# Performance work log

Measured on AMD Instinct MI355X. Metric: run time of the kernel, lower is better.

The kernel has to match this reference:

```python
import jax, jax.numpy as jnp
import numpy as np

N = 1 << 20  # total rows
D = 64       # feature dim
HALF = N // 2


def setup_inputs() -> dict:
    key = jax.random.key(0)
    k_data, k_part, k_perm = jax.random.split(key, 3)
    data = jax.random.normal(k_data, (N, D), dtype=jnp.float32)
    # exactly HALF zeros and HALF ones, randomly interleaved -> static partition sizes
    labels = jnp.concatenate([jnp.zeros(HALF, jnp.int32), jnp.ones(HALF, jnp.int32)])
    partitions = jax.random.permutation(k_part, labels)
    # destination rows: a random permutation of [0, N) split between the two partitions
    perm = jax.random.permutation(k_perm, jnp.arange(N, dtype=jnp.int32))
    index0 = perm[:HALF]
    index1 = perm[HALF:]
    return {"data": data, "partitions": partitions, "index0": index0, "index1": index1}


def reference(data, partitions, index0, index1):
    n0 = index0.shape[0]  # static size of partition 0 (by construction)
    # dynamic_partition: stable sort by label puts partition-0 rows (in original
    # order) first, then partition-1 rows (in original order).
    order = jnp.argsort(partitions, stable=True)  # [N] gather indices
    part0 = data[order[:n0]]   # rows with partitions == 0, original order
    part1 = data[order[n0:]]   # rows with partitions == 1, original order
    # dynamic_stitch: out[index0[i]] = part0[i]; out[index1[j]] = part1[j]
    out = jnp.zeros((n0 + index1.shape[0], data.shape[1]), dtype=data.dtype)
    out = out.at[index0].set(part0)
    out = out.at[index1].set(part1)
    return out
```

## Files before the change

### kernel.cpp

```cpp
#include <hip/hip_runtime.h>

#define GROUP 256

typedef float f4 __attribute__((ext_vector_type(4)));

__global__ __launch_bounds__(256)
void dps_count(const int* __restrict__ parts, int n, int* __restrict__ group_sums) {
    const int t = threadIdx.x;
    const int w = t >> 6;
    const int n4 = n >> 2;
    const int4* p4 = reinterpret_cast<const int4*>(parts);
    #pragma unroll
    for (int it = 0; it < 16; ++it) {
        int i4 = blockIdx.x * 4096 + it * 256 + t;
        int s = 0;
        if (i4 < n4) {
            int4 v = p4[i4];
            s = v.x + v.y + v.z + v.w;
        }
        #pragma unroll
        for (int off = 32; off >= 1; off >>= 1) s += __shfl_down(s, off, 64);
        if ((t & 63) == 0) {
            int g = blockIdx.x * 64 + it * 4 + w;
            int ngroups = (n + GROUP - 1) / GROUP;
            if (g < ngroups) group_sums[g] = s;
        }
    }
}

__global__ __launch_bounds__(256)
void dps_scan(int* __restrict__ gs, int nb) {
    __shared__ int lds[256];
    const int t = threadIdx.x;
    int v[16];
    int s = 0;
    #pragma unroll
    for (int k = 0; k < 16; ++k) {
        int idx = t * 16 + k;
        v[k] = (idx < nb) ? gs[idx] : 0;
        s += v[k];
    }
    lds[t] = s;
    __syncthreads();
    for (int off = 1; off < 256; off <<= 1) {
        int add = (t >= off) ? lds[t - off] : 0;
        __syncthreads();
        lds[t] += add;
        __syncthreads();
    }
    int run = lds[t] - s;
    #pragma unroll
    for (int k = 0; k < 16; ++k) {
        int idx = t * 16 + k;
        if (idx < nb) gs[idx] = run;
        run += v[k];
    }
}

__global__ __launch_bounds__(256)
void dps_fused(const f4* __restrict__ data4,
               const int* __restrict__ parts,
               const int* __restrict__ index0,
               const int* __restrict__ index1,
               const int* __restrict__ group_excl,
               int n,
               f4* __restrict__ out4) {
    __shared__ int lds [256];
    __shared__ int ldsd[256];
    const int t    = threadIdx.x;
    const int base = blockIdx.x * GROUP;
    const int i    = base + t;

    int p = (i < n) ? parts[i] : 0;
    lds[t] = p;
    __syncthreads();
    for (int off = 1; off < 256; off <<= 1) {
        int add = (t >= off) ? lds[t - off] : 0;
        __syncthreads();
        lds[t] += add;
        __syncthreads();
    }
    int ones_excl = group_excl[blockIdx.x] + (lds[t] - p);
    if (i < n) {
        ldsd[t] = p ? index1[ones_excl] : index0[i - ones_excl];
    }
    __syncthreads();

    const f4* src = data4 + ((long)base << 4);
    const int q  = t & 15;
    const int r0 = t >> 4;
    if (base + GROUP <= n) {
        #pragma unroll
        for (int it = 0; it < 16; ++it) {
            int r = it * 16 + r0;
            f4 v = __builtin_nontemporal_load(src + (r << 4) + q);
            long dr = (long)ldsd[r];
            __builtin_nontemporal_store(v, out4 + (dr << 4) + q);
        }
    } else {
        for (int it = 0; it < 16; ++it) {
            int r = it * 16 + r0;
            if (base + r < n) {
                f4 v = src[(r << 4) + q];
                out4[((long)ldsd[r] << 4) + q] = v;
            }
        }
    }
}

extern "C" void kernel_launch(void* const* d_in, const int* in_sizes, int n_in,
                              void* d_out, int out_size, void* d_ws, size_t ws_size,
                              hipStream_t stream) {
    const float* data   = (const float*)d_in[0];
    const int*   parts  = (const int*)d_in[1];
    const int*   index0 = (const int*)d_in[2];
    const int*   index1 = (const int*)d_in[3];
    const int n = in_sizes[1];

    int* group_sums = (int*)d_ws;

    const int ngroups = (n + GROUP - 1) / GROUP;
    const int cblocks = (n / 4 + 4095) / 4096;

    dps_count<<<cblocks, 256, 0, stream>>>(parts, n, group_sums);
    dps_scan <<<1,       256, 0, stream>>>(group_sums, ngroups);
    dps_fused<<<ngroups, 256, 0, stream>>>((const f4*)data, parts, index0, index1,
                                           group_sums, n, (f4*)d_out);
}
```

Before: 122.4 us.

## Fuse count, scan and scatter into one cooperative kernel with grid sync

```diff
diff --git a/kernel.cpp b/kernel.cpp
--- a/kernel.cpp
+++ b/kernel.cpp
@@ -1,109 +1,107 @@
 #include <hip/hip_runtime.h>
+#include <hip/hip_cooperative_groups.h>
 
-#define GROUP 256
+namespace cg = cooperative_groups;
 
 typedef float f4 __attribute__((ext_vector_type(4)));
 
-__global__ __launch_bounds__(256)
-void dps_count(const int* __restrict__ parts, int n, int* __restrict__ group_sums) {
-    const int t = threadIdx.x;
-    const int w = t >> 6;
-    const int n4 = n >> 2;
-    const int4* p4 = reinterpret_cast<const int4*>(parts);
-    #pragma unroll
-    for (int it = 0; it < 16; ++it) {
-        int i4 = blockIdx.x * 4096 + it * 256 + t;
-        int s = 0;
-        if (i4 < n4) {
-            int4 v = p4[i4];
-            s = v.x + v.y + v.z + v.w;
-        }
-        #pragma unroll
-        for (int off = 32; off >= 1; off >>= 1) s += __shfl_down(s, off, 64);
-        if ((t & 63) == 0) {
-            int g = blockIdx.x * 64 + it * 4 + w;
-            int ngroups = (n + GROUP - 1) / GROUP;
-            if (g < ngroups) group_sums[g] = s;
+#define NBLK 1024
+#define NTHR 256
+#define RPB  (NTHR * 4)
+
+__global__ __launch_bounds__(NTHR, 4)
+void dps_all(const f4* __restrict__ data4,
+             const int* __restrict__ parts,
+             const int* __restrict__ index0,
+             const int* __restrict__ index1,
+             int* __restrict__ bs,
+             int n,
+             f4* __restrict__ out4) {
+    __shared__ int lds[NTHR];
+    __shared__ int dstL[RPB];
+    const int t    = threadIdx.x;
+    const int b    = blockIdx.x;
+    const int base = b * RPB;
+
+    int v0 = 0, v1 = 0, v2 = 0, v3 = 0;
+    {
+        int i0 = base + t * 4;
+        if (i0 + 3 < n) {
+            int4 p = reinterpret_cast<const int4*>(parts)[(base >> 2) + t];
+            v0 = p.x; v1 = p.y; v2 = p.z; v3 = p.w;
+        } else {
+            if (i0 + 0 < n) v0 = parts[i0 + 0];
+            if (i0 + 1 < n) v1 = parts[i0 + 1];
+            if (i0 + 2 < n) v2 = parts[i0 + 2];
+            if (i0 + 3 < n) v3 = parts[i0 + 3];
         }
     }
-}
-
-__global__ __launch_bounds__(256)
-void dps_scan(int* __restrict__ gs, int nb) {
-    __shared__ int lds[256];
-    const int t = threadIdx.x;
-    int v[16];
-    int s = 0;
-    #pragma unroll
-    for (int k = 0; k < 16; ++k) {
-        int idx = t * 16 + k;
-        v[k] = (idx < nb) ? gs[idx] : 0;
-        s += v[k];
-    }
+    int s = v0 + v1 + v2 + v3;
     lds[t] = s;
     __syncthreads();
-    for (int off = 1; off < 256; off <<= 1) {
+    for (int off = 1; off < NTHR; off <<= 1) {
         int add = (t >= off) ? lds[t - off] : 0;
         __syncthreads();
         lds[t] += add;
         __syncthreads();
     }
-    int run = lds[t] - s;
-    #pragma unroll
-    for (int k = 0; k < 16; ++k) {
-        int idx = t * 16 + k;
-        if (idx < nb) gs[idx] = run;
-        run += v[k];
+    const int texcl = lds[t] - s;
+    if (t == 0) bs[b] = lds[NTHR - 1];
+    __threadfence();
+    cg::this_grid().sync();
+
+    int partial = 0;
+    {
+        int4 q = reinterpret_cast<const int4*>(bs)[t];
+        int e = t * 4;
+        if (e + 0 < b) partial += q.x;
+        if (e + 1 < b) partial += q.y;
+        if (e + 2 < b) partial += q.z;
+        if (e + 3 < b) partial += q.w;
     }
-}
-
-__global__ __launch_bounds__(256)
-void dps_fused(const f4* __restrict__ data4,
-               const int* __restrict__ parts,
-               const int* __restrict__ index0,
-               const int* __restrict__ index1,
-               const int* __restrict__ group_excl,
-               int n,
-               f4* __restrict__ out4) {
-    __shared__ int lds [256];
-    __shared__ int ldsd[256];
-    const int t    = threadIdx.x;
-    const int base = blockIdx.x * GROUP;
-    const int i    = base + t;
-
-    int p = (i < n) ? parts[i] : 0;
-    lds[t] = p;
     __syncthreads();
-    for (int off = 1; off < 256; off <<= 1) {
-        int add = (t >= off) ? lds[t - off] : 0;
-        __syncthreads();
-        lds[t] += add;
+    lds[t] = partial;
+    __syncthreads();
+    for (int off = NTHR / 2; off > 0; off >>= 1) {
+        if (t < off) lds[t] += lds[t + off];
         __syncthreads();
     }
-    int ones_excl = group_excl[blockIdx.x] + (lds[t] - p);
-    if (i < n) {
-        ldsd[t] = p ? index1[ones_excl] : index0[i - ones_excl];
+    const int block_excl = lds[0];
+
+    {
+        int ones = block_excl + texcl;
+        int i0 = base + t * 4;
+        int d0 = 0, d1 = 0, d2 = 0, d3 = 0;
+        if (i0 + 0 < n) { d0 = v0 ? index1[ones] : index0[i0 + 0 - ones]; ones += v0; }
+        if (i0 + 1 < n) { d1 = v1 ? index1[ones] : index0[i0 + 1 - ones]; ones += v1; }
+        if (i0 + 2 < n) { d2 = v2 ? index1[ones] : index0[i0 + 2 - ones]; ones += v2; }
+        if (i0 + 3 < n) { d3 = v3 ? index1[ones] : index0[i0 + 3 - ones]; ones += v3; }
+        dstL[t * 4 + 0] = d0; dstL[t * 4 + 1] = d1;
+        dstL[t * 4 + 2] = d2; dstL[t * 4 + 3] = d3;
     }
     __syncthreads();
 
     const f4* src = data4 + ((long)base << 4);
-    const int q  = t & 15;
-    const int r0 = t >> 4;
-    if (base + GROUP <= n) {
+    if (base + RPB <= n) {
         #pragma unroll
         for (int it = 0; it < 16; ++it) {
-            int r = it * 16 + r0;
-            f4 v = __builtin_nontemporal_load(src + (r << 4) + q);
-            long dr = (long)ldsd[r];
-            __builtin_nontemporal_store(v, out4 + (dr << 4) + q);
+            f4 w[4]; long o[4];
+            #pragma unroll
+            for (int k = 0; k < 4; ++k) {
+                int id = it * 1024 + k * 256 + t;
+                w[k] = __builtin_nontemporal_load(src + id);
+                int row = id >> 4, q = id & 15;
+                o[k] = ((long)dstL[row] << 4) + q;
+            }
+            #pragma unroll
+            for (int k = 0; k < 4; ++k) out4[o[k]] = w[k];
         }
     } else {
-        for (int it = 0; it < 16; ++it) {
-            int r = it * 16 + r0;
-            if (base + r < n) {
-                f4 v = src[(r << 4) + q];
-                out4[((long)ldsd[r] << 4) + q] = v;
-            }
+        int rem = (n - base) * 16;
+        for (int id = t; id < rem; id += NTHR) {
+            int row = id >> 4, q = id & 15;
+            f4 w = src[id];
+            out4[((long)dstL[row] << 4) + q] = w;
         }
     }
 }
@@ -111,19 +109,15 @@
 extern "C" void kernel_launch(void* const* d_in, const int* in_sizes, int n_in,
                               void* d_out, int out_size, void* d_ws, size_t ws_size,
                               hipStream_t stream) {
-    const float* data   = (const float*)d_in[0];
-    const int*   parts  = (const int*)d_in[1];
-    const int*   index0 = (const int*)d_in[2];
-    const int*   index1 = (const int*)d_in[3];
-    const int n = in_sizes[1];
+    const f4*  data4  = (const f4*)d_in[0];
+    const int* parts  = (const int*)d_in[1];
+    const int* index0 = (const int*)d_in[2];
+    const int* index1 = (const int*)d_in[3];
+    f4*        out4   = (f4*)d_out;
+    int n = in_sizes[1];
+    int* bs = (int*)d_ws;
 
-    int* group_sums = (int*)d_ws;
-
-    const int ngroups = (n + GROUP - 1) / GROUP;
-    const int cblocks = (n / 4 + 4095) / 4096;
-
-    dps_count<<<cblocks, 256, 0, stream>>>(parts, n, group_sums);
-    dps_scan <<<1,       256, 0, stream>>>(group_sums, ngroups);
-    dps_fused<<<ngroups, 256, 0, stream>>>((const f4*)data, parts, index0, index1,
-                                           group_sums, n, (f4*)d_out);
+    void* args[] = { (void*)&data4, (void*)&parts, (void*)&index0, (void*)&index1,
+                     (void*)&bs, (void*)&n, (void*)&out4 };
+    hipLaunchCooperativeKernel((void*)dps_all, dim3(NBLK), dim3(NTHR), args, 0, stream);
 }
```

Result: slower. 193.2 us (+57.8%).
